# Performance work log

Hardware: AMD Instinct MI355X
Metric: run time of the kernel (lower is better)

## Reference

```python
import jax, jax.numpy as jnp
import numpy as np

N = 64       # number of sites / qubits
CHI = 32     # bond dimension chi_max
D = 2        # physical dim (== label dim l)
BATCH = 262144
STD = 0.001  # init noise, matches MPS.initialize_params


def setup_inputs() -> dict:
    key = jax.random.key(0)
    kx, k0, kc, kn = jax.random.split(key, 4)
    # X: [N, batch, d] -- each X[i] contracts with site i's physical leg
    X = jax.random.normal(kx, (N, BATCH, D), dtype=jnp.float32)
    # core0: (d, chi), one-hot column 0 plus noise
    core0 = jnp.zeros((D, CHI), jnp.float32).at[:, 0].set(1.0)
    core0 = core0 + STD * jax.random.normal(k0, (D, CHI), dtype=jnp.float32)
    # middle cores: (N-1, chi, d, chi), identity stacked over d plus noise
    eye = jnp.eye(CHI, dtype=jnp.float32)                      # (chi, chi)
    mid = jnp.broadcast_to(eye[:, None, :], (CHI, D, CHI))     # (chi, d, chi)
    cores = jnp.broadcast_to(mid, (N - 1, CHI, D, CHI))
    cores = cores + STD * jax.random.normal(kc, (N - 1, CHI, D, CHI), dtype=jnp.float32)
    # coreN: (chi, d), one-hot row 0 plus noise
    coreN = jnp.zeros((CHI, D), jnp.float32).at[0].set(1.0)
    coreN = coreN + STD * jax.random.normal(kn, (CHI, D), dtype=jnp.float32)
    return {"X": X, "core0": core0, "cores": cores, "coreN": coreN}


def reference(X, core0, cores, coreN):
    # Sequential MPS chain contraction:
    #   v <- X[0] @ core0                       (batch, chi)
    #   v <- einsum('ab,bqc,aq->ac', v, core_i, X[i])   for i = 1..N-1
    #   out = |v @ coreN|                       (batch, l)
    v0 = jnp.einsum('aq,qc->ac', X[0], core0)  # (B, chi)

    def step(v, inp):
        x, core = inp  # x: (B, d), core: (chi, d, chi)
        # contract bond then physical leg, keeping only (B, chi) resident
        v_new = jnp.einsum('ab,bqc,aq->ac', v, core, x)
        return v_new, None

    v, _ = jax.lax.scan(step, v0, (X[1:], cores))
    out = jnp.einsum('ac,cq->aq', v, coreN)    # (B, l)
    return jnp.abs(out)
```

## Files before the change

kernel.cpp:

```cpp
#include <hip/hip_runtime.h>

#define BATCH 262144
#define NSITES 64
#define KPAD 40

typedef __attribute__((ext_vector_type(8))) short short8;
typedef __attribute__((ext_vector_type(4))) float f32x4;

__device__ __forceinline__ unsigned cvt_pk_bf16(float lo, float hi) {
  unsigned r;
  asm("v_cvt_pk_bf16_f32 %0, %1, %2" : "=v"(r) : "v"(lo), "v"(hi));
  return r;
}

__device__ __forceinline__ int qinv(int chi) {
  return (((chi >> 2) & 3) << 3) | (((chi >> 4) & 1) << 2) | (chi & 3);
}

struct Smem {
  alignas(16) short A[2][2][32][KPAD];
  alignas(16) float c0p[2][32];
  alignas(16) float cNp[32][2];
};

__device__ __forceinline__ void stage_load(const float* __restrict__ cores, int s, int tid,
                                           float sv[2][4]) {
#pragma unroll
  for (int r = 0; r < 2; ++r) {
    int V = tid + 256 * r;
    int c = V & 31, m = (V >> 5) & 1, b0 = (V >> 6) * 4;
    const float* p = cores + (s - 1) * 2048 + b0 * 64 + m * 32 + c;
    sv[r][0] = p[0];
    sv[r][1] = p[64];
    sv[r][2] = p[128];
    sv[r][3] = p[192];
  }
}

__device__ __forceinline__ void stage_write(short (*Ab)[32][KPAD], int tid,
                                            const float sv[2][4]) {
#pragma unroll
  for (int r = 0; r < 2; ++r) {
    int V = tid + 256 * r;
    int c = V & 31, m = (V >> 5) & 1, b0 = (V >> 6) * 4;
    float f0 = sv[r][0] - ((c == b0 + 0) ? 1.0f : 0.0f);
    float f1 = sv[r][1] - ((c == b0 + 1) ? 1.0f : 0.0f);
    float f2 = sv[r][2] - ((c == b0 + 2) ? 1.0f : 0.0f);
    float f3 = sv[r][3] - ((c == b0 + 3) ? 1.0f : 0.0f);
    unsigned p0 = cvt_pk_bf16(f0, f1);
    unsigned p1 = cvt_pk_bf16(f2, f3);
    int kq = (((b0 >> 2) & 3) << 3) | (((b0 >> 4) & 1) << 2);
    unsigned* dst = (unsigned*)&Ab[m][c][kq];
    dst[0] = p0;
    dst[1] = p1;
  }
}

__global__ __launch_bounds__(256, 4) void mps_chain_kernel(
    const float* __restrict__ X, const float* __restrict__ core0,
    const float* __restrict__ cores, const float* __restrict__ coreN,
    float* __restrict__ out) {
  __shared__ Smem sm;
  const int tid = threadIdx.x;
  const int lane = tid & 63;
  const int wave = tid >> 6;
  const int col = lane & 15;
  const int g = lane >> 4;
  const int abase = blockIdx.x * 256 + wave * 64;

  float sv[2][4];
  stage_load(cores, 1, tid, sv);
  if (tid < 64) {
    int m = tid >> 5, chi = tid & 31;
    sm.c0p[m][qinv(chi)] = core0[tid];
  } else if (tid < 128) {
    int t = tid - 64;
    int chi = t >> 1, cc = t & 1;
    sm.cNp[qinv(chi)][cc] = coreN[t];
  }
  stage_write(sm.A[0], tid, sv);
  __syncthreads();

  float v[4][8];
  const f32x4 c00 = *(const f32x4*)&sm.c0p[0][8 * g];
  const f32x4 c01 = *(const f32x4*)&sm.c0p[0][8 * g + 4];
  const f32x4 c10 = *(const f32x4*)&sm.c0p[1][8 * g];
  const f32x4 c11 = *(const f32x4*)&sm.c0p[1][8 * g + 4];
#pragma unroll
  for (int j = 0; j < 4; ++j) {
    const float2 xj = *(const float2*)(X + 2 * (size_t)(abase + j * 16 + col));
#pragma unroll
    for (int t = 0; t < 4; ++t) {
      v[j][t] = xj.x * c00[t] + xj.y * c10[t];
      v[j][4 + t] = xj.x * c01[t] + xj.y * c11[t];
    }
  }

  for (int s = 1; s < NSITES; ++s) {
    const int buf = (s - 1) & 1;
    if (s < NSITES - 1) stage_load(cores, s + 1, tid, sv);

    float2 x[4];
#pragma unroll
    for (int j = 0; j < 4; ++j)
      x[j] = *(const float2*)(X + 2 * ((size_t)s * BATCH + abase + j * 16 + col));

    const short8 A00 = *(const short8*)&sm.A[buf][0][col][8 * g];
    const short8 A01 = *(const short8*)&sm.A[buf][0][16 + col][8 * g];
    const short8 A10 = *(const short8*)&sm.A[buf][1][col][8 * g];
    const short8 A11 = *(const short8*)&sm.A[buf][1][16 + col][8 * g];

#pragma unroll
    for (int j = 0; j < 4; ++j) {
      union {
        short8 s8;
        unsigned u[4];
      } vb;
      vb.u[0] = cvt_pk_bf16(v[j][0], v[j][1]);
      vb.u[1] = cvt_pk_bf16(v[j][2], v[j][3]);
      vb.u[2] = cvt_pk_bf16(v[j][4], v[j][5]);
      vb.u[3] = cvt_pk_bf16(v[j][6], v[j][7]);
      const f32x4 z = {0.f, 0.f, 0.f, 0.f};
      f32x4 r0lo = __builtin_amdgcn_mfma_f32_16x16x32_bf16(A00, vb.s8, z, 0, 0, 0);
      f32x4 r0hi = __builtin_amdgcn_mfma_f32_16x16x32_bf16(A01, vb.s8, z, 0, 0, 0);
      f32x4 r1lo = __builtin_amdgcn_mfma_f32_16x16x32_bf16(A10, vb.s8, z, 0, 0, 0);
      f32x4 r1hi = __builtin_amdgcn_mfma_f32_16x16x32_bf16(A11, vb.s8, z, 0, 0, 0);
      const float s01 = x[j].x + x[j].y;
#pragma unroll
      for (int t = 0; t < 4; ++t) {
        v[j][t] = s01 * v[j][t] + x[j].x * r0lo[t] + x[j].y * r1lo[t];
        v[j][4 + t] = s01 * v[j][4 + t] + x[j].x * r0hi[t] + x[j].y * r1hi[t];
      }
    }

    if (s < NSITES - 1) stage_write(sm.A[buf ^ 1], tid, sv);
    __syncthreads();
  }

#pragma unroll
  for (int j = 0; j < 4; ++j) {
    float p0 = 0.f, p1 = 0.f;
#pragma unroll
    for (int u = 0; u < 4; ++u) {
      const f32x4 cn = *(const f32x4*)&sm.cNp[8 * g + 2 * u][0];
      p0 += v[j][2 * u] * cn[0] + v[j][2 * u + 1] * cn[2];
      p1 += v[j][2 * u] * cn[1] + v[j][2 * u + 1] * cn[3];
    }
    p0 += __shfl_xor(p0, 16);
    p0 += __shfl_xor(p0, 32);
    p1 += __shfl_xor(p1, 16);
    p1 += __shfl_xor(p1, 32);
    if (g == 0) {
      const int a = abase + j * 16 + col;
      out[2 * a] = fabsf(p0);
      out[2 * a + 1] = fabsf(p1);
    }
  }
}

extern "C" void kernel_launch(void* const* d_in, const int* in_sizes, int n_in,
                              void* d_out, int out_size, void* d_ws, size_t ws_size,
                              hipStream_t stream) {
  const float* X = (const float*)d_in[0];
  const float* core0 = (const float*)d_in[1];
  const float* cores = (const float*)d_in[2];
  const float* coreN = (const float*)d_in[3];
  float* out = (float*)d_out;
  dim3 grid(BATCH / 256);
  dim3 block(256);
  hipLaunchKernelGGL(mps_chain_kernel, grid, block, 0, stream, X, core0, cores, coreN, out);
}
```

Baseline: 110.9 us.

## Prepack core deltas to bf16 in a separate kernel and drop LDS staging

Adds a small pre-kernel that subtracts the identity from each core, converts to bf16 and writes the result in MFMA fragment order to workspace. The main kernel then loads A fragments straight from global memory (L2-resident) into registers, software-pipelined one site ahead. It also prefetches X two sites ahead, removing the shared-memory staging and the per-site __syncthreads. The cost is an extra kernel launch and the reliance on cache hits for the repeated fragment loads across blocks.

```diff
diff --git a/kernel.cpp b/kernel.cpp
--- a/kernel.cpp
+++ b/kernel.cpp
@@ -1,8 +1,8 @@
 #include <hip/hip_runtime.h>
+#include <hip/hip_bf16.h>
 
 #define BATCH 262144
 #define NSITES 64
-#define KPAD 40
 
 typedef __attribute__((ext_vector_type(8))) short short8;
 typedef __attribute__((ext_vector_type(4))) float f32x4;
@@ -13,54 +13,30 @@
   return r;
 }
 
+__device__ __forceinline__ int qmap(int k) {
+  return (((k >> 2) & 1) << 4) | (((k >> 3) & 3) << 2) | (k & 3);
+}
 __device__ __forceinline__ int qinv(int chi) {
   return (((chi >> 2) & 3) << 3) | (((chi >> 4) & 1) << 2) | (chi & 3);
 }
 
-struct Smem {
-  alignas(16) short A[2][2][32][KPAD];
-  alignas(16) float c0p[2][32];
-  alignas(16) float cNp[32][2];
-};
-
-__device__ __forceinline__ void stage_load(const float* __restrict__ cores, int s, int tid,
-                                           float sv[2][4]) {
-#pragma unroll
-  for (int r = 0; r < 2; ++r) {
-    int V = tid + 256 * r;
-    int c = V & 31, m = (V >> 5) & 1, b0 = (V >> 6) * 4;
-    const float* p = cores + (s - 1) * 2048 + b0 * 64 + m * 32 + c;
-    sv[r][0] = p[0];
-    sv[r][1] = p[64];
-    sv[r][2] = p[128];
-    sv[r][3] = p[192];
-  }
-}
-
-__device__ __forceinline__ void stage_write(short (*Ab)[32][KPAD], int tid,
-                                            const float sv[2][4]) {
-#pragma unroll
-  for (int r = 0; r < 2; ++r) {
-    int V = tid + 256 * r;
-    int c = V & 31, m = (V >> 5) & 1, b0 = (V >> 6) * 4;
-    float f0 = sv[r][0] - ((c == b0 + 0) ? 1.0f : 0.0f);
-    float f1 = sv[r][1] - ((c == b0 + 1) ? 1.0f : 0.0f);
-    float f2 = sv[r][2] - ((c == b0 + 2) ? 1.0f : 0.0f);
-    float f3 = sv[r][3] - ((c == b0 + 3) ? 1.0f : 0.0f);
-    unsigned p0 = cvt_pk_bf16(f0, f1);
-    unsigned p1 = cvt_pk_bf16(f2, f3);
-    int kq = (((b0 >> 2) & 3) << 3) | (((b0 >> 4) & 1) << 2);
-    unsigned* dst = (unsigned*)&Ab[m][c][kq];
-    dst[0] = p0;
-    dst[1] = p1;
-  }
+__global__ void pack_E(const float* __restrict__ cores, unsigned short* __restrict__ Ep) {
+  int idx = blockIdx.x * 256 + threadIdx.x;
+  if (idx >= (NSITES - 1) * 2048) return;
+  int s = idx >> 11;
+  int r = idx & 2047;
+  int b = r >> 6;
+  int m = (r >> 5) & 1;
+  int c = r & 31;
+  float f = cores[idx] - ((b == c) ? 1.0f : 0.0f);
+  __hip_bfloat16 h = __float2bfloat16(f);
+  Ep[((s * 2 + m) * 32 + c) * 32 + qinv(b)] = *(unsigned short*)&h;
 }
 
 __global__ __launch_bounds__(256, 4) void mps_chain_kernel(
     const float* __restrict__ X, const float* __restrict__ core0,
-    const float* __restrict__ cores, const float* __restrict__ coreN,
+    const float* __restrict__ coreN, const unsigned short* __restrict__ Ep,
     float* __restrict__ out) {
-  __shared__ Smem sm;
   const int tid = threadIdx.x;
   const int lane = tid & 63;
   const int wave = tid >> 6;
@@ -68,47 +44,44 @@
   const int g = lane >> 4;
   const int abase = blockIdx.x * 256 + wave * 64;
 
-  float sv[2][4];
-  stage_load(cores, 1, tid, sv);
-  if (tid < 64) {
-    int m = tid >> 5, chi = tid & 31;
-    sm.c0p[m][qinv(chi)] = core0[tid];
-  } else if (tid < 128) {
-    int t = tid - 64;
-    int chi = t >> 1, cc = t & 1;
-    sm.cNp[qinv(chi)][cc] = coreN[t];
-  }
-  stage_write(sm.A[0], tid, sv);
-  __syncthreads();
+  float c0[2][8];
+#pragma unroll
+  for (int m = 0; m < 2; ++m)
+#pragma unroll
+    for (int t = 0; t < 8; ++t) c0[m][t] = core0[m * 32 + qmap(8 * g + t)];
 
   float v[4][8];
-  const f32x4 c00 = *(const f32x4*)&sm.c0p[0][8 * g];
-  const f32x4 c01 = *(const f32x4*)&sm.c0p[0][8 * g + 4];
-  const f32x4 c10 = *(const f32x4*)&sm.c0p[1][8 * g];
-  const f32x4 c11 = *(const f32x4*)&sm.c0p[1][8 * g + 4];
 #pragma unroll
   for (int j = 0; j < 4; ++j) {
     const float2 xj = *(const float2*)(X + 2 * (size_t)(abase + j * 16 + col));
 #pragma unroll
-    for (int t = 0; t < 4; ++t) {
-      v[j][t] = xj.x * c00[t] + xj.y * c10[t];
-      v[j][4 + t] = xj.x * c01[t] + xj.y * c11[t];
-    }
+    for (int t = 0; t < 8; ++t) v[j][t] = xj.x * c0[0][t] + xj.y * c0[1][t];
   }
 
+  const short8* EpV = (const short8*)Ep;
+  const int rA = col, rB = col + 16;
+#define FRAG(s, m, row) EpV[(((s)*2 + (m)) * 32 + (row)) * 4 + g]
+
+  short8 Ac0 = FRAG(0, 0, rA), Ac1 = FRAG(0, 0, rB);
+  short8 Ac2 = FRAG(0, 1, rA), Ac3 = FRAG(0, 1, rB);
+
+  float2 xc[4], xm[4];
+#pragma unroll
+  for (int j = 0; j < 4; ++j) {
+    xc[j] = *(const float2*)(X + 2 * ((size_t)1 * BATCH + abase + j * 16 + col));
+    xm[j] = *(const float2*)(X + 2 * ((size_t)2 * BATCH + abase + j * 16 + col));
+  }
+
+#pragma unroll 1
   for (int s = 1; s < NSITES; ++s) {
-    const int buf = (s - 1) & 1;
-    if (s < NSITES - 1) stage_load(cores, s + 1, tid, sv);
-
-    float2 x[4];
+    const int sn = (s < NSITES - 1) ? s : NSITES - 2;
+    short8 An0 = FRAG(sn, 0, rA), An1 = FRAG(sn, 0, rB);
+    short8 An2 = FRAG(sn, 1, rA), An3 = FRAG(sn, 1, rB);
+    const size_t sx = (s + 2 < NSITES) ? (size_t)(s + 2) : (size_t)(NSITES - 1);
+    float2 xn[4];
 #pragma unroll
     for (int j = 0; j < 4; ++j)
-      x[j] = *(const float2*)(X + 2 * ((size_t)s * BATCH + abase + j * 16 + col));
-
-    const short8 A00 = *(const short8*)&sm.A[buf][0][col][8 * g];
-    const short8 A01 = *(const short8*)&sm.A[buf][0][16 + col][8 * g];
-    const short8 A10 = *(const short8*)&sm.A[buf][1][col][8 * g];
-    const short8 A11 = *(const short8*)&sm.A[buf][1][16 + col][8 * g];
+      xn[j] = *(const float2*)(X + 2 * (sx * BATCH + abase + j * 16 + col));
 
 #pragma unroll
     for (int j = 0; j < 4; ++j) {
@@ -121,30 +94,38 @@
       vb.u[2] = cvt_pk_bf16(v[j][4], v[j][5]);
       vb.u[3] = cvt_pk_bf16(v[j][6], v[j][7]);
       const f32x4 z = {0.f, 0.f, 0.f, 0.f};
-      f32x4 r0lo = __builtin_amdgcn_mfma_f32_16x16x32_bf16(A00, vb.s8, z, 0, 0, 0);
-      f32x4 r0hi = __builtin_amdgcn_mfma_f32_16x16x32_bf16(A01, vb.s8, z, 0, 0, 0);
-      f32x4 r1lo = __builtin_amdgcn_mfma_f32_16x16x32_bf16(A10, vb.s8, z, 0, 0, 0);
-      f32x4 r1hi = __builtin_amdgcn_mfma_f32_16x16x32_bf16(A11, vb.s8, z, 0, 0, 0);
-      const float s01 = x[j].x + x[j].y;
+      f32x4 r0lo = __builtin_amdgcn_mfma_f32_16x16x32_bf16(Ac0, vb.s8, z, 0, 0, 0);
+      f32x4 r0hi = __builtin_amdgcn_mfma_f32_16x16x32_bf16(Ac1, vb.s8, z, 0, 0, 0);
+      f32x4 r1lo = __builtin_amdgcn_mfma_f32_16x16x32_bf16(Ac2, vb.s8, z, 0, 0, 0);
+      f32x4 r1hi = __builtin_amdgcn_mfma_f32_16x16x32_bf16(Ac3, vb.s8, z, 0, 0, 0);
+      const float x0 = xc[j].x, x1 = xc[j].y;
+      const float s01 = x0 + x1;
 #pragma unroll
       for (int t = 0; t < 4; ++t) {
-        v[j][t] = s01 * v[j][t] + x[j].x * r0lo[t] + x[j].y * r1lo[t];
-        v[j][4 + t] = s01 * v[j][4 + t] + x[j].x * r0hi[t] + x[j].y * r1hi[t];
+        v[j][t] = s01 * v[j][t] + x0 * r0lo[t] + x1 * r1lo[t];
+        v[j][4 + t] = s01 * v[j][4 + t] + x0 * r0hi[t] + x1 * r1hi[t];
       }
     }
 
-    if (s < NSITES - 1) stage_write(sm.A[buf ^ 1], tid, sv);
-    __syncthreads();
+    Ac0 = An0; Ac1 = An1; Ac2 = An2; Ac3 = An3;
+#pragma unroll
+    for (int j = 0; j < 4; ++j) { xc[j] = xm[j]; xm[j] = xn[j]; }
   }
+#undef FRAG
 
+  float cN[8][2];
+#pragma unroll
+  for (int t = 0; t < 8; ++t) {
+    cN[t][0] = coreN[qmap(8 * g + t) * 2 + 0];
+    cN[t][1] = coreN[qmap(8 * g + t) * 2 + 1];
+  }
 #pragma unroll
   for (int j = 0; j < 4; ++j) {
     float p0 = 0.f, p1 = 0.f;
 #pragma unroll
-    for (int u = 0; u < 4; ++u) {
-      const f32x4 cn = *(const f32x4*)&sm.cNp[8 * g + 2 * u][0];
-      p0 += v[j][2 * u] * cn[0] + v[j][2 * u + 1] * cn[2];
-      p1 += v[j][2 * u] * cn[1] + v[j][2 * u + 1] * cn[3];
+    for (int t = 0; t < 8; ++t) {
+      p0 += v[j][t] * cN[t][0];
+      p1 += v[j][t] * cN[t][1];
     }
     p0 += __shfl_xor(p0, 16);
     p0 += __shfl_xor(p0, 32);
@@ -166,7 +147,10 @@
   const float* cores = (const float*)d_in[2];
   const float* coreN = (const float*)d_in[3];
   float* out = (float*)d_out;
-  dim3 grid(BATCH / 256);
-  dim3 block(256);
-  hipLaunchKernelGGL(mps_chain_kernel, grid, block, 0, stream, X, core0, cores, coreN, out);
+  unsigned short* Ep = (unsigned short*)d_ws;
+
+  hipLaunchKernelGGL(pack_E, dim3(((NSITES - 1) * 2048 + 255) / 256), dim3(256), 0, stream,
+                     cores, Ep);
+  hipLaunchKernelGGL(mps_chain_kernel, dim3(BATCH / 256), dim3(256), 0, stream, X, core0,
+                     coreN, Ep, out);
 }
```

Result: slower. 136.4 us (+23.0%).
